# Kernel optimization log

Measured on AMD Instinct MI355X. Metric: run time of the kernel, lower is better.

## Reference

```python
import jax, jax.numpy as jnp
import numpy as np

N = 100000
E = 1600000
IN = 128
OUT = 64
H = 4
NEG_SLOPE = 0.2


def setup_inputs() -> dict:
    key = jax.random.key(0)
    k1, k2, k3, k4, k5, k6 = jax.random.split(key, 6)
    Z = jax.random.normal(k1, (N, IN), dtype=jnp.float32)
    row = jax.random.randint(k2, (E,), 0, N, dtype=jnp.int32)
    col = jax.random.randint(k3, (E,), 0, N, dtype=jnp.int32)
    # xavier-normal-ish scaled params
    W = jax.random.normal(k4, (OUT * H, IN), dtype=jnp.float32) * (2.0 / np.sqrt(IN + OUT * H))
    b = jnp.zeros((OUT * H,), dtype=jnp.float32)
    a_l = jax.random.normal(k5, (1, OUT, H), dtype=jnp.float32) * 0.1
    a_r = jax.random.normal(k6, (1, OUT, H), dtype=jnp.float32) * 0.1
    return {"Z": Z, "row": row, "col": col, "W": W, "b": b, "a_l": a_l, "a_r": a_r}


def reference(Z, row, col, W, b, a_l, a_r):
    # Linear projection + reshape to [N, OUT, H]
    Zp = (Z @ W.T + b).reshape(Z.shape[0], OUT, H)
    # per-node attention logits [N, H]
    e_l = (Zp * a_l).sum(axis=1)
    e_r = (Zp * a_r).sum(axis=1)
    # edge scores (SDDMM-like gather) [E, H]
    e = e_l[row] + e_r[col]
    a = jnp.where(e > 0, e, NEG_SLOPE * e)  # LeakyReLU
    # segment softmax over incoming edges of each destination row
    m = jax.ops.segment_max(a, row, num_segments=N)  # [N, H]; -inf for empty rows
    m = jnp.where(jnp.isfinite(m), m, 0.0)
    a_exp = jnp.exp(a - m[row])
    denom = jax.ops.segment_sum(a_exp, row, num_segments=N)  # [N, H]
    denom = jnp.where(denom == 0, 1.0, denom)
    att = a_exp / denom[row]  # [E, H]
    # bspmm: out[i, :, h] = sum_{edges e with row=i} att[e, h] * Zp[col[e], :, h]
    msgs = att[:, None, :] * Zp[col]  # [E, OUT, H]
    out = jax.ops.segment_sum(msgs, row, num_segments=N)  # [N, OUT, H]
    return out
```

## Files before the change

kernel.cpp:

```cpp
#include <hip/hip_runtime.h>
#include <math.h>

#define IN_F 128
#define C_TOT 256
#define NEG_SLOPE 0.2f
#define CAP 64
#define NPB 256
#define MAXPB 5120
#define CL 16

typedef __attribute__((ext_vector_type(8))) short short8;
typedef __attribute__((ext_vector_type(4))) float f32x4;

static __device__ __forceinline__ ushort f2bf(float f) {
    unsigned u = __float_as_uint(f);
    unsigned r = (u + 0x7FFF + ((u >> 16) & 1)) >> 16;
    return (ushort)r;
}
static __device__ __forceinline__ float bf2f_lo(unsigned w) { return __uint_as_float(w << 16); }
static __device__ __forceinline__ float bf2f_hi(unsigned w) { return __uint_as_float(w & 0xFFFF0000u); }

__global__ __launch_bounds__(512) void part1_kernel(
    const int* __restrict__ row, const int* __restrict__ col,
    int* __restrict__ gb, int2* __restrict__ part, int E, int NB)
{
    __shared__ int hist[512], cur[512], start[512];
    const int t = threadIdx.x;
    const int base = blockIdx.x * 8192;
    hist[t] = 0;
    __syncthreads();
#pragma unroll
    for (int i = 0; i < 16; ++i) {
        int e = base + i * 512 + t;
        if (e < E) atomicAdd(&hist[row[e] >> 8], 1);
    }
    __syncthreads();
    if (t < NB) start[t] = hist[t] ? atomicAdd(&gb[t * CL], hist[t]) : 0;
    cur[t] = 0;
    __syncthreads();
#pragma unroll
    for (int i = 0; i < 16; ++i) {
        int e = base + i * 512 + t;
        if (e < E) {
            int r = row[e];
            int b = r >> 8;
            int p = start[b] + atomicAdd(&cur[b], 1);
            if (p < MAXPB) part[(size_t)b * MAXPB + p] = make_int2(r, col[e]);
        }
    }
}

__global__ __launch_bounds__(512) void part2_kernel(
    const int2* __restrict__ part, const int* __restrict__ gb,
    int* __restrict__ cnt, int* __restrict__ ebuf, int N, int NB)
{
    __shared__ int lcnt[NPB];
    const int b = blockIdx.x;
    const int t = threadIdx.x;
    if (t < NPB) lcnt[t] = 0;
    __syncthreads();
    int cb = gb[b * CL];
    if (cb > MAXPB) cb = MAXPB;
    const int2* p = part + (size_t)b * MAXPB;
    for (int i = t; i < cb; i += 512) {
        int2 e = p[i];
        int s = atomicAdd(&lcnt[e.x & (NPB - 1)], 1);
        if (s < CAP) ebuf[(size_t)e.x * CAP + s] = e.y;
    }
    __syncthreads();
    if (t < NPB) {
        int n = b * NPB + t;
        if (n < N) cnt[n] = lcnt[t];
    }
}

__global__ __launch_bounds__(512) void gemm_kernel(
    const float* __restrict__ Z, const float* __restrict__ W,
    const float* __restrict__ bias, const float* __restrict__ a_l,
    const float* __restrict__ a_r, ushort* __restrict__ Zp,
    float* __restrict__ el, float* __restrict__ er, int N)
{
    __shared__ ushort Ws[C_TOT * IN_F];
    const int t = threadIdx.x;
#pragma unroll
    for (int j = 0; j < 8; ++j) {
        int baddr = (j * 512 + t) * 16;
        int r = baddr >> 8;
        int cb = baddr & 255;
        const float* wsrc = W + (size_t)r * IN_F + (cb >> 1);
        float4 a0 = *(const float4*)wsrc;
        float4 a1 = *(const float4*)(wsrc + 4);
        short8 f;
        f[0] = (short)f2bf(a0.x); f[1] = (short)f2bf(a0.y);
        f[2] = (short)f2bf(a0.z); f[3] = (short)f2bf(a0.w);
        f[4] = (short)f2bf(a1.x); f[5] = (short)f2bf(a1.y);
        f[6] = (short)f2bf(a1.z); f[7] = (short)f2bf(a1.w);
        *(short8*)((char*)Ws + r * 256 + (cb ^ ((r & 7) << 4))) = f;
    }
    __syncthreads();

    const int wave = t >> 6, lane = t & 63;
    const int lr = lane & 15, lq = lane >> 4;
    const int row0 = (blockIdx.x * 8 + wave) * 16;
    if (row0 >= N) return;

    short8 afrag[4];
    const bool rowok = (row0 + lr) < N;
    const float* zrow = Z + (size_t)(row0 + lr) * IN_F + lq * 8;
#pragma unroll
    for (int ks = 0; ks < 4; ++ks) {
        short8 f = (short8)0;
        if (rowok) {
            float4 a0 = *(const float4*)(zrow + ks * 32);
            float4 a1 = *(const float4*)(zrow + ks * 32 + 4);
            f[0] = (short)f2bf(a0.x); f[1] = (short)f2bf(a0.y);
            f[2] = (short)f2bf(a0.z); f[3] = (short)f2bf(a0.w);
            f[4] = (short)f2bf(a1.x); f[5] = (short)f2bf(a1.y);
            f[6] = (short)f2bf(a1.z); f[7] = (short)f2bf(a1.w);
        }
        afrag[ks] = f;
    }

    f32x4 acc[16];
#pragma unroll
    for (int ct = 0; ct < 16; ++ct) acc[ct] = (f32x4)0.f;

    const int swz = (lr & 7) << 4;
#pragma unroll
    for (int ks = 0; ks < 4; ++ks) {
#pragma unroll
        for (int ct = 0; ct < 16; ++ct) {
            short8 bfrag = *(const short8*)((const char*)Ws +
                           (ct * 16 + lr) * 256 + (((ks * 64 + lq * 16)) ^ swz));
            acc[ct] = __builtin_amdgcn_mfma_f32_16x16x32_bf16(afrag[ks], bfrag, acc[ct], 0, 0, 0);
        }
    }

    float elp[4] = {0.f, 0.f, 0.f, 0.f}, erp[4] = {0.f, 0.f, 0.f, 0.f};
#pragma unroll
    for (int ct = 0; ct < 16; ++ct) {
        const int colc = ct * 16 + lr;
        const float bb = bias[colc];
        const float al = a_l[colc];
        const float ar = a_r[colc];
#pragma unroll
        for (int r = 0; r < 4; ++r) {
            const int rr = row0 + lq * 4 + r;
            float v = acc[ct][r] + bb;
            if (rr < N) Zp[(size_t)rr * C_TOT + colc] = f2bf(v);
            elp[r] += v * al;
            erp[r] += v * ar;
        }
    }
#pragma unroll
    for (int r = 0; r < 4; ++r) {
        elp[r] += __shfl_xor(elp[r], 4); elp[r] += __shfl_xor(elp[r], 8);
        erp[r] += __shfl_xor(erp[r], 4); erp[r] += __shfl_xor(erp[r], 8);
    }
    if (lr < 4) {
#pragma unroll
        for (int r = 0; r < 4; ++r) {
            const int rr = row0 + lq * 4 + r;
            if (rr < N) {
                el[rr * 4 + lr] = elp[r];
                er[rr * 4 + lr] = erp[r];
            }
        }
    }
}

__global__ __launch_bounds__(256) void agg_kernel(
    const int* __restrict__ cnt, const int* __restrict__ ebuf,
    const float* __restrict__ el, const float* __restrict__ er,
    const ushort* __restrict__ Zp, float* __restrict__ out, int N)
{
    __shared__ int    cS[16][2][17];
    __shared__ float4 wS[16][2][17];
    const int tid = threadIdx.x;
    const int sub = tid >> 4, fl = tid & 15;
    const int n = blockIdx.x * 16 + sub;

    int beg = 0, deg = 0;
    float4 el4 = make_float4(0.f, 0.f, 0.f, 0.f);
    if (n < N) {
        beg = n * CAP;
        deg = cnt[n];
        if (deg > CAP) deg = CAP;
        el4 = *(const float4*)&el[(size_t)n * 4];
    }
    int nch = (deg + 15) >> 4;
    {
        int m = nch;
        m = max(m, __shfl_xor(m, 16));
        m = max(m, __shfl_xor(m, 32));
        nch = m;
    }

    float acc[16];
#pragma unroll
    for (int k = 0; k < 16; ++k) acc[k] = 0.f;
    float ds0 = 0.f, ds1 = 0.f, ds2 = 0.f, ds3 = 0.f;

#define STAGE(CH, BUF) do {                                                   \
        int _o = (CH) * 16 + fl;                                              \
        bool _v = _o < deg;                                                   \
        int _i = beg + _o;                                                    \
        int _c = _v ? ebuf[_i] : -1;                                          \
        float4 _w = make_float4(0.f, 0.f, 0.f, 0.f);                          \
        if (_v) {                                                             \
            float4 _e = *(const float4*)&er[(size_t)_c * 4];                  \
            float _a0 = el4.x + _e.x; _a0 = _a0 > 0.f ? _a0 : NEG_SLOPE * _a0;\
            float _a1 = el4.y + _e.y; _a1 = _a1 > 0.f ? _a1 : NEG_SLOPE * _a1;\
            float _a2 = el4.z + _e.z; _a2 = _a2 > 0.f ? _a2 : NEG_SLOPE * _a2;\
            float _a3 = el4.w + _e.w; _a3 = _a3 > 0.f ? _a3 : NEG_SLOPE * _a3;\
            _w.x = __expf(fminf(_a0, 60.f));                                  \
            _w.y = __expf(fminf(_a1, 60.f));                                  \
            _w.z = __expf(fminf(_a2, 60.f));                                  \
            _w.w = __expf(fminf(_a3, 60.f));                                  \
            ds0 += _w.x; ds1 += _w.y; ds2 += _w.z; ds3 += _w.w;               \
        }                                                                     \
        cS[sub][BUF][fl] = _c;                                                \
        wS[sub][BUF][fl] = _w;                                                \
    } while (0)

#define PROCESS(BUF) do {                                                     \
        _Pragma("unroll")                                                     \
        for (int j = 0; j < 16; ++j) {                                        \
            int _c = cS[sub][BUF][j];                                         \
            if (_c >= 0) {                                                    \
                float4 _w = wS[sub][BUF][j];                                  \
                const ushort* _zr = Zp + (size_t)_c * C_TOT + fl * 16;        \
                uint4 _A = *(const uint4*)_zr;                                \
                uint4 _B = *(const uint4*)(_zr + 8);                          \
                unsigned _pw[8] = {_A.x, _A.y, _A.z, _A.w,                    \
                                   _B.x, _B.y, _B.z, _B.w};                   \
                _Pragma("unroll")                                             \
                for (int wd = 0; wd < 8; ++wd) {                              \
                    int k0 = wd * 2;                                          \
                    float wl = (k0 & 2) ? _w.z : _w.x;                        \
                    float wh = (k0 & 2) ? _w.w : _w.y;                        \
                    acc[k0]     += wl * bf2f_lo(_pw[wd]);                     \
                    acc[k0 + 1] += wh * bf2f_hi(_pw[wd]);                     \
                }                                                             \
            }                                                                 \
        }                                                                     \
    } while (0)

    if (nch > 0) {
        STAGE(0, 0);
        int buf = 0;
        for (int ch = 0; ch < nch; ++ch) {
            if (ch + 1 < nch) STAGE(ch + 1, buf ^ 1);
            __builtin_amdgcn_wave_barrier();
            PROCESS(buf);
            __builtin_amdgcn_wave_barrier();
            buf ^= 1;
        }
    }
#undef STAGE
#undef PROCESS

#pragma unroll
    for (int d = 1; d < 16; d <<= 1) {
        ds0 += __shfl_xor(ds0, d); ds1 += __shfl_xor(ds1, d);
        ds2 += __shfl_xor(ds2, d); ds3 += __shfl_xor(ds3, d);
    }

    if (n < N) {
        float4 iv;
        iv.x = ds0 > 0.f ? 1.f / ds0 : 1.f;
        iv.y = ds1 > 0.f ? 1.f / ds1 : 1.f;
        iv.z = ds2 > 0.f ? 1.f / ds2 : 1.f;
        iv.w = ds3 > 0.f ? 1.f / ds3 : 1.f;
        float* orow = out + (size_t)n * C_TOT + fl * 16;
#pragma unroll
        for (int g = 0; g < 4; ++g) {
            float4 o;
            o.x = acc[g * 4 + 0] * iv.x;
            o.y = acc[g * 4 + 1] * iv.y;
            o.z = acc[g * 4 + 2] * iv.z;
            o.w = acc[g * 4 + 3] * iv.w;
            *(float4*)(orow + g * 4) = o;
        }
    }
}

extern "C" void kernel_launch(void* const* d_in, const int* in_sizes, int n_in,
                              void* d_out, int out_size, void* d_ws, size_t ws_size,
                              hipStream_t stream)
{
    const float* Z   = (const float*)d_in[0];
    const int*   row = (const int*)d_in[1];
    const int*   col = (const int*)d_in[2];
    const float* W   = (const float*)d_in[3];
    const float* b   = (const float*)d_in[4];
    const float* a_l = (const float*)d_in[5];
    const float* a_r = (const float*)d_in[6];
    float* out = (float*)d_out;
    const int N = in_sizes[0] / IN_F;
    const int E = in_sizes[1];
    const int NB = (N + NPB - 1) / NPB;

    char* ws = (char*)d_ws;
    size_t o = 0;
    auto alloc = [&](size_t bytes) -> void* {
        void* p = ws + o;
        o = (o + bytes + 255) & ~(size_t)255;
        return p;
    };
    ushort* Zp   = (ushort*)alloc((size_t)N * C_TOT * 2);
    float*  el   = (float*)alloc((size_t)N * 4 * 4);
    float*  er   = (float*)alloc((size_t)N * 4 * 4);
    int*    cnt  = (int*)alloc((size_t)N * 4);
    int*    ebuf = (int*)alloc((size_t)N * CAP * 4);
    int*    gb   = (int*)alloc((size_t)NB * CL * 4);
    int2*   part = (int2*)alloc((size_t)NB * MAXPB * 8);

    (void)hipMemsetAsync(gb, 0, (size_t)NB * CL * 4, stream);

    part1_kernel<<<(E + 8191) / 8192, 512, 0, stream>>>(row, col, gb, part, E, NB);
    part2_kernel<<<NB, 512, 0, stream>>>(part, gb, cnt, ebuf, N, NB);

    gemm_kernel<<<(N + 127) / 128, 512, 0, stream>>>(Z, W, b, a_l, a_r,
                                                     Zp, el, er, N);

    agg_kernel<<<(N + 15) / 16, 256, 0, stream>>>(cnt, ebuf, el, er, Zp, out, N);
}
```

Baseline: 212.9 us.

## Replace global-atomic bucket partition with per-block slots and prefix-scan compaction

The edge-bucketing pass no longer reserves space with global atomics. Each block instead writes its edges into a fixed per-(bucket, block) slot region and records a histogram entry. The second pass scans those counts in shared memory and binary-searches to gather edges. Edges are also packed into 4 bytes (row low bits plus col) instead of 8 bytes, and the memset is dropped. This costs a larger, sparsely filled partition buffer with a hard per-slot cap of 64, and adds a 512-wide scan plus a binary search per edge.

```diff
diff --git a/kernel.cpp b/kernel.cpp
--- a/kernel.cpp
+++ b/kernel.cpp
@@ -6,8 +6,9 @@
 #define NEG_SLOPE 0.2f
 #define CAP 64
 #define NPB 256
-#define MAXPB 5120
-#define CL 16
+#define EPB 8192
+#define CAPB 64
+#define MAXBLK 512
 
 typedef __attribute__((ext_vector_type(8))) short short8;
 typedef __attribute__((ext_vector_type(4))) float f32x4;
@@ -22,50 +23,75 @@
 
 __global__ __launch_bounds__(512) void part1_kernel(
     const int* __restrict__ row, const int* __restrict__ col,
-    int* __restrict__ gb, int2* __restrict__ part, int E, int NB)
-{
-    __shared__ int hist[512], cur[512], start[512];
+    int* __restrict__ ghist, unsigned* __restrict__ part,
+    int E, int NB, int NBLK)
+{
+    __shared__ int lh[512];
     const int t = threadIdx.x;
-    const int base = blockIdx.x * 8192;
-    hist[t] = 0;
-    __syncthreads();
-#pragma unroll
-    for (int i = 0; i < 16; ++i) {
-        int e = base + i * 512 + t;
-        if (e < E) atomicAdd(&hist[row[e] >> 8], 1);
-    }
-    __syncthreads();
-    if (t < NB) start[t] = hist[t] ? atomicAdd(&gb[t * CL], hist[t]) : 0;
-    cur[t] = 0;
-    __syncthreads();
-#pragma unroll
-    for (int i = 0; i < 16; ++i) {
+    const int blk = blockIdx.x;
+    const int base = blk * EPB;
+    lh[t] = 0;
+    __syncthreads();
+#pragma unroll
+    for (int i = 0; i < EPB / 512; ++i) {
         int e = base + i * 512 + t;
         if (e < E) {
             int r = row[e];
+            int c = col[e];
             int b = r >> 8;
-            int p = start[b] + atomicAdd(&cur[b], 1);
-            if (p < MAXPB) part[(size_t)b * MAXPB + p] = make_int2(r, col[e]);
-        }
-    }
+            int s = atomicAdd(&lh[b], 1);
+            if (s < CAPB)
+                part[((size_t)b * NBLK + blk) * CAPB + s] =
+                    ((unsigned)(r & 255) << 24) | (unsigned)c;
+        }
+    }
+    __syncthreads();
+    if (t < NB) ghist[t * NBLK + blk] = lh[t];
 }
 
 __global__ __launch_bounds__(512) void part2_kernel(
-    const int2* __restrict__ part, const int* __restrict__ gb,
-    int* __restrict__ cnt, int* __restrict__ ebuf, int N, int NB)
-{
+    const unsigned* __restrict__ part, const int* __restrict__ ghist,
+    int* __restrict__ cnt, int* __restrict__ ebuf, int N, int NBLK)
+{
+    __shared__ int scnt[MAXBLK], ipref[MAXBLK];
     __shared__ int lcnt[NPB];
     const int b = blockIdx.x;
     const int t = threadIdx.x;
     if (t < NPB) lcnt[t] = 0;
-    __syncthreads();
-    int cb = gb[b * CL];
-    if (cb > MAXPB) cb = MAXPB;
-    const int2* p = part + (size_t)b * MAXPB;
-    for (int i = t; i < cb; i += 512) {
-        int2 e = p[i];
-        int s = atomicAdd(&lcnt[e.x & (NPB - 1)], 1);
-        if (s < CAP) ebuf[(size_t)e.x * CAP + s] = e.y;
+    {
+        int c0 = 0;
+        if (t < NBLK) {
+            c0 = ghist[b * NBLK + t];
+            if (c0 > CAPB) c0 = CAPB;
+        }
+        scnt[t] = c0;
+        if (t + 512 < MAXBLK) { scnt[t + 512] = 0; }
+    }
+    __syncthreads();
+    int own = scnt[t];
+    ipref[t] = own;
+    __syncthreads();
+    for (int d = 1; d < 512; d <<= 1) {
+        int v = (t >= d) ? ipref[t - d] : 0;
+        __syncthreads();
+        ipref[t] += v;
+        __syncthreads();
+    }
+    const int total = ipref[511];
+
+    const unsigned* pb = part + (size_t)b * NBLK * CAPB;
+    for (int i = t; i < total; i += 512) {
+        int lo = 0, hi = NBLK - 1;
+        while (lo < hi) {
+            int mid = (lo + hi) >> 1;
+            if (ipref[mid] > i) hi = mid; else lo = mid + 1;
+        }
+        int off = i - (lo ? ipref[lo - 1] : 0);
+        unsigned e = pb[lo * CAPB + off];
+        int rlow = (int)(e >> 24);
+        int c = (int)(e & 0xFFFFFFu);
+        int s = atomicAdd(&lcnt[rlow], 1);
+        if (s < CAP) ebuf[(size_t)(b * NPB + rlow) * CAP + s] = c;
     }
     __syncthreads();
     if (t < NPB) {
@@ -300,6 +326,7 @@
     const int N = in_sizes[0] / IN_F;
     const int E = in_sizes[1];
     const int NB = (N + NPB - 1) / NPB;
+    const int NBLK = (E + EPB - 1) / EPB;
 
     char* ws = (char*)d_ws;
     size_t o = 0;
@@ -308,18 +335,16 @@
         o = (o + bytes + 255) & ~(size_t)255;
         return p;
     };
-    ushort* Zp   = (ushort*)alloc((size_t)N * C_TOT * 2);
-    float*  el   = (float*)alloc((size_t)N * 4 * 4);
-    float*  er   = (float*)alloc((size_t)N * 4 * 4);
-    int*    cnt  = (int*)alloc((size_t)N * 4);
-    int*    ebuf = (int*)alloc((size_t)N * CAP * 4);
-    int*    gb   = (int*)alloc((size_t)NB * CL * 4);
-    int2*   part = (int2*)alloc((size_t)NB * MAXPB * 8);
-
-    (void)hipMemsetAsync(gb, 0, (size_t)NB * CL * 4, stream);
-
-    part1_kernel<<<(E + 8191) / 8192, 512, 0, stream>>>(row, col, gb, part, E, NB);
-    part2_kernel<<<NB, 512, 0, stream>>>(part, gb, cnt, ebuf, N, NB);
+    ushort*   Zp    = (ushort*)alloc((size_t)N * C_TOT * 2);
+    float*    el    = (float*)alloc((size_t)N * 4 * 4);
+    float*    er    = (float*)alloc((size_t)N * 4 * 4);
+    int*      cnt   = (int*)alloc((size_t)N * 4);
+    int*      ebuf  = (int*)alloc((size_t)N * CAP * 4);
+    int*      ghist = (int*)alloc((size_t)NB * NBLK * 4);
+    unsigned* part  = (unsigned*)alloc((size_t)NB * NBLK * CAPB * 4);
+
+    part1_kernel<<<NBLK, 512, 0, stream>>>(row, col, ghist, part, E, NB, NBLK);
+    part2_kernel<<<NB, 512, 0, stream>>>(part, ghist, cnt, ebuf, N, NBLK);
 
     gemm_kernel<<<(N + 127) / 128, 512, 0, stream>>>(Z, W, b, a_l, a_r,
                                                      Zp, el, er, N);
```

Result: faster. 201.4 us (-5.4%).
